# Kernel optimization log

Hardware: AMD Instinct MI355X
Metric: run time of the kernel (lower is better)

## Reference

```python
import jax, jax.numpy as jnp
import numpy as np

B, S, D, H = 2, 2048, 2048, 16
DEPTH = D // H


def setup_inputs() -> dict:
    key = jax.random.key(0)
    ks = jax.random.split(key, 12)
    std = 1.0 / np.sqrt(D)
    mk = lambda k, shape: (jax.random.uniform(k, shape, jnp.float32) * 2 - 1) * std
    # causal additive mask: 1.0 where future position (masked), 0.0 elsewhere
    mask = jnp.triu(jnp.ones((S, S), jnp.float32), k=1)[None, None]
    return {
        "q": jax.random.normal(ks[0], (B, S, D), jnp.float32),
        "k": jax.random.normal(ks[1], (B, S, D), jnp.float32),
        "v": jax.random.normal(ks[2], (B, S, D), jnp.float32),
        "mask": mask,
        "wq_w": mk(ks[3], (D, D)), "wq_b": mk(ks[4], (D,)),
        "wk_w": mk(ks[5], (D, D)), "wk_b": mk(ks[6], (D,)),
        "wv_w": mk(ks[7], (D, D)), "wv_b": mk(ks[8], (D,)),
        "dense_w": mk(ks[9], (D, D)), "dense_b": mk(ks[10], (D,)),
    }


def split_heads(x):
    # [B,S,D] -> [B,H,S,depth]
    b, s, _ = x.shape
    return x.reshape(b, s, H, DEPTH).transpose(0, 2, 1, 3)


def reference(q, k, v, mask, wq_w, wq_b, wk_w, wk_b, wv_w, wv_b, dense_w, dense_b):
    # torch Linear: y = x @ W.T + b
    qh = split_heads(q @ wq_w.T + wq_b)
    kh = split_heads(k @ wk_w.T + wk_b)
    vh = split_heads(v @ wv_w.T + wv_b)
    scale = 1.0 / jnp.sqrt(jnp.asarray(DEPTH, jnp.float32))
    logits = jnp.einsum("bhqd,bhkd->bhqk", qh, kh) * scale
    logits = logits + mask * (-1e9)
    weights = jax.nn.softmax(logits, axis=-1)  # dropout is identity in eval
    out = jnp.einsum("bhqk,bhkd->bhqd", weights, vh)
    out = out.transpose(0, 2, 1, 3).reshape(q.shape[0], -1, D)
    return out @ dense_w.T + dense_b
```

## Files before the change

kernel.cpp:

```cpp
#include <hip/hip_runtime.h>
#include <hip/hip_bf16.h>


typedef __bf16 bf16x8 __attribute__((ext_vector_type(8)));
typedef float f32x4 __attribute__((ext_vector_type(4)));
typedef float f32x16 __attribute__((ext_vector_type(16)));
typedef unsigned short u16;
typedef unsigned int u32;

#define DEV static __device__ __forceinline__

DEV void gload_lds16(const void* g, void* l) {
  __builtin_amdgcn_global_load_lds(
      (const __attribute__((address_space(1))) void*)g,
      (__attribute__((address_space(3))) void*)l, 16, 0, 0);
}

DEV f32x4 mfma16(bf16x8 a, bf16x8 b, f32x4 c) {
  return __builtin_amdgcn_mfma_f32_16x16x32_bf16(a, b, c, 0, 0, 0);
}

DEV f32x16 mfma32(bf16x8 a, bf16x8 b, f32x16 c) {
  return __builtin_amdgcn_mfma_f32_32x32x16_bf16(a, b, c, 0, 0, 0);
}

DEV u16 f2bf(float x) {
  return __builtin_bit_cast(u16, __float2bfloat16(x));
}

DEV u32 pack2(float lo, float hi_) {
  return (u32)f2bf(lo) | ((u32)f2bf(hi_) << 16);
}

#define BAR() __builtin_amdgcn_s_barrier()

__global__ void __launch_bounds__(256) conv_f32_bf16(
    const float* __restrict__ in, u16* __restrict__ out) {
  const size_t i = ((size_t)blockIdx.x * 256 + threadIdx.x) * 4;
  const float4 v = *reinterpret_cast<const float4*>(in + i);
  ushort4 o;
  o.x = f2bf(v.x); o.y = f2bf(v.y); o.z = f2bf(v.z); o.w = f2bf(v.w);
  *reinterpret_cast<ushort4*>(out + i) = o;
}

__global__ void __launch_bounds__(256) conv_all(
    const float* __restrict__ s0, const float* __restrict__ s1,
    const float* __restrict__ s2, const float* __restrict__ s3,
    const float* __restrict__ s4, const float* __restrict__ s5,
    const float* __restrict__ s6,
    u16* __restrict__ d0, u16* __restrict__ d1, u16* __restrict__ d2,
    u16* __restrict__ d3, u16* __restrict__ d4, u16* __restrict__ d5,
    u16* __restrict__ d6, const size_t nact, const size_t nw) {
  const int j = blockIdx.y;
  const size_t i = ((size_t)blockIdx.x * 256 + threadIdx.x) * 4;
  const float* s; u16* d; size_t n;
  switch (j) {
    case 0: s = s0; d = d0; n = nact; break;
    case 1: s = s1; d = d1; n = nact; break;
    case 2: s = s2; d = d2; n = nact; break;
    case 3: s = s3; d = d3; n = nw; break;
    case 4: s = s4; d = d4; n = nw; break;
    case 5: s = s5; d = d5; n = nw; break;
    default: s = s6; d = d6; n = nw; break;
  }
  if (i >= n) return;
  const float4 v = *reinterpret_cast<const float4*>(s + i);
  ushort4 o;
  o.x = f2bf(v.x); o.y = f2bf(v.y); o.z = f2bf(v.z); o.w = f2bf(v.w);
  *reinterpret_cast<ushort4*>(d + i) = o;
}

#define GK 2048

DEV void gemm128_core(const u16* __restrict__ A, const u16* __restrict__ Bw,
                      const float* __restrict__ bias, void* __restrict__ Cout,
                      const int m0, const int n0, const int N,
                      const int out_f32, u16* AsB, u16* BsB) {
  const int tid = threadIdx.x;
  const int lane = tid & 63;
  const int wid = tid >> 6;
  const int wr = wid >> 1, wc = wid & 1;
  const int g = lane >> 4;
  const int r16 = lane & 15;

  int offA[2], offB[2], dstE[2];
#pragma unroll
  for (int rr = 0; rr < 2; ++rr) {
    const int G = rr * 256 + tid;
    const int rp = G >> 3;
    const int s = (G & 7) ^ (rp & 7);
    const int row = rp * 2 + (s >> 2);
    const int ch = s & 3;
    offA[rr] = (m0 + row) * GK + ch * 8;
    offB[rr] = (n0 + row) * GK + ch * 8;
    dstE[rr] = rr * 2048 + wid * 512;
  }

#define STAGE_A(kt, kh) do {                                              \
    u16* base_ = AsB + (((kt) & 1) * 2 + (kh)) * 4096;                    \
    const int go_ = (kt) * 64 + (kh) * 32;                                \
    gload_lds16(A + (size_t)(offA[0] + go_), base_ + dstE[0]);            \
    gload_lds16(A + (size_t)(offA[1] + go_), base_ + dstE[1]);            \
  } while (0)
#define STAGE_B(kt, kh) do {                                              \
    u16* base_ = BsB + (((kt) & 1) * 2 + (kh)) * 4096;                    \
    const int go_ = (kt) * 64 + (kh) * 32;                                \
    gload_lds16(Bw + (size_t)(offB[0] + go_), base_ + dstE[0]);           \
    gload_lds16(Bw + (size_t)(offB[1] + go_), base_ + dstE[1]);           \
  } while (0)
#define READ_A(MH, buf) do {                                              \
    _Pragma("unroll") for (int i_ = 0; i_ < 2; ++i_) {                    \
      const int row_ = wr * 64 + ((MH) * 2 + i_) * 16 + r16;              \
      const int rp_ = row_ >> 1;                                          \
      const int sl_ = (((row_ & 1) << 2) | g) ^ (rp_ & 7);                \
      const int off_ = rp_ * 64 + sl_ * 8;                                \
      af[i_][0] = *(const bf16x8*)(AsB + ((buf) * 2 + 0) * 4096 + off_);  \
      af[i_][1] = *(const bf16x8*)(AsB + ((buf) * 2 + 1) * 4096 + off_);  \
    } } while (0)
#define READ_B(NH, buf, bf) do {                                          \
    _Pragma("unroll") for (int j_ = 0; j_ < 2; ++j_) {                    \
      const int row_ = wc * 64 + ((NH) * 2 + j_) * 16 + r16;              \
      const int rp_ = row_ >> 1;                                          \
      const int sl_ = (((row_ & 1) << 2) | g) ^ (rp_ & 7);                \
      const int off_ = rp_ * 64 + sl_ * 8;                                \
      bf[j_][0] = *(const bf16x8*)(BsB + ((buf) * 2 + 0) * 4096 + off_);  \
      bf[j_][1] = *(const bf16x8*)(BsB + ((buf) * 2 + 1) * 4096 + off_);  \
    } } while (0)
#define MFMA_Q(MH, NH, bf) do {                                           \
    __builtin_amdgcn_s_setprio(1);                                        \
    _Pragma("unroll") for (int i_ = 0; i_ < 2; ++i_)                      \
    _Pragma("unroll") for (int j_ = 0; j_ < 2; ++j_) {                    \
      f32x4 c_ = acc[(MH) * 2 + i_][(NH) * 2 + j_];                       \
      c_ = mfma16(af[i_][0], bf[j_][0], c_);                              \
      c_ = mfma16(af[i_][1], bf[j_][1], c_);                              \
      acc[(MH) * 2 + i_][(NH) * 2 + j_] = c_;                             \
    }                                                                     \
    __builtin_amdgcn_s_setprio(0);                                        \
  } while (0)

  f32x4 acc[4][4];
#pragma unroll
  for (int i = 0; i < 4; ++i)
#pragma unroll
    for (int j = 0; j < 4; ++j) acc[i][j] = {0.f, 0.f, 0.f, 0.f};

  bf16x8 af[2][2], bf0[2][2], bf1[2][2];

  STAGE_B(0, 0); STAGE_B(0, 1); STAGE_A(0, 0); STAGE_A(0, 1);
  STAGE_B(1, 0); STAGE_B(1, 1);
  asm volatile("s_waitcnt vmcnt(4)" ::: "memory");
  BAR();

  for (int it = 0; it < 16; ++it) {
    const bool tail = (it == 15);
    const int t0 = 2 * it, t1 = t0 + 1;
    READ_A(0, 0); READ_B(0, 0, bf0);
    STAGE_A(t1, 0);
    BAR(); MFMA_Q(0, 0, bf0); BAR();
    READ_B(1, 0, bf1);
    STAGE_A(t1, 1);
    BAR(); MFMA_Q(0, 1, bf1); BAR();
    READ_A(1, 0);
    if (!tail) STAGE_B(t0 + 2, 0);
    BAR(); MFMA_Q(1, 0, bf0); BAR();
    if (!tail) {
      STAGE_B(t0 + 2, 1);
      asm volatile("s_waitcnt vmcnt(4)" ::: "memory");
    } else {
      asm volatile("s_waitcnt vmcnt(0)" ::: "memory");
    }
    BAR(); MFMA_Q(1, 1, bf1); BAR();
    READ_A(0, 1); READ_B(0, 1, bf0);
    if (!tail) STAGE_A(t0 + 2, 0);
    BAR(); MFMA_Q(0, 0, bf0); BAR();
    READ_B(1, 1, bf1);
    if (!tail) STAGE_A(t0 + 2, 1);
    BAR(); MFMA_Q(0, 1, bf1); BAR();
    READ_A(1, 1);
    if (!tail) STAGE_B(t1 + 2, 0);
    BAR(); MFMA_Q(1, 0, bf0); BAR();
    if (!tail) {
      STAGE_B(t1 + 2, 1);
      asm volatile("s_waitcnt vmcnt(4)" ::: "memory");
    } else {
      asm volatile("s_waitcnt vmcnt(0)" ::: "memory");
    }
    BAR(); MFMA_Q(1, 1, bf1); BAR();
  }

  const int rbase = m0 + wr * 64 + g * 4;
  const int cb = n0 + wc * 64 + r16;
#pragma unroll
  for (int i = 0; i < 4; ++i) {
#pragma unroll
    for (int j = 0; j < 4; ++j) {
      const int c = cb + j * 16;
      const float bv = bias[c];
#pragma unroll
      for (int r = 0; r < 4; ++r) {
        const float v = acc[i][j][r] + bv;
        const size_t idx = (size_t)(rbase + i * 16 + r) * N + c;
        if (out_f32) ((float*)Cout)[idx] = v;
        else ((u16*)Cout)[idx] = f2bf(v);
      }
    }
  }
#undef STAGE_A
#undef STAGE_B
#undef READ_A
#undef READ_B
#undef MFMA_Q
}

__global__ void __launch_bounds__(256, 2) gemm_qkv3(
    const u16* __restrict__ A0, const u16* __restrict__ A1,
    const u16* __restrict__ A2, const u16* __restrict__ W0,
    const u16* __restrict__ W1, const u16* __restrict__ W2,
    const float* __restrict__ b0, const float* __restrict__ b1,
    const float* __restrict__ b2, u16* __restrict__ C0,
    u16* __restrict__ C1, u16* __restrict__ C2) {
  __shared__ u16 AsB[4 * 4096];
  __shared__ u16 BsB[4 * 4096];
  const int xcd = blockIdx.x & 7;
  const int t = blockIdx.x >> 3;
  const int which = t >> 6;
  const int r = t & 63;
  const int m0 = (xcd * 4 + (r >> 4)) << 7;
  const int n0 = (r & 15) << 7;
  const u16* A = which == 0 ? A0 : which == 1 ? A1 : A2;
  const u16* W = which == 0 ? W0 : which == 1 ? W1 : W2;
  const float* bb = which == 0 ? b0 : which == 1 ? b1 : b2;
  u16* C = which == 0 ? C0 : which == 1 ? C1 : C2;
  gemm128_core(A, W, bb, C, m0, n0, 2048, 0, AsB, BsB);
}

__global__ void __launch_bounds__(256, 2) gemm_one(
    const u16* __restrict__ A, const u16* __restrict__ Bw,
    const float* __restrict__ bias, void* __restrict__ Cout,
    const int out_f32) {
  __shared__ u16 AsB[4 * 4096];
  __shared__ u16 BsB[4 * 4096];
  const int xcd = blockIdx.x & 7;
  const int t = blockIdx.x >> 3;
  const int m0 = (xcd * 4 + (t >> 4)) << 7;
  const int n0 = (t & 15) << 7;
  gemm128_core(A, Bw, bias, Cout, m0, n0, 2048, out_f32, AsB, BsB);
}

#define SEQ 2048
#define DMODEL 2048
#define DH 128
#define QBLK 128
#define KBLK 64
#define C1 0.12751744f
#define THR_RAW 62.73f

__global__ void __launch_bounds__(256, 2) flash_attn(
    const u16* __restrict__ Qh, const u16* __restrict__ Kh,
    const u16* __restrict__ Vh, u16* __restrict__ O) {
  __shared__ u16 Ks[2][KBLK * DH];
  __shared__ u16 Vt[DH * KBLK];

  const int tid = threadIdx.x;
  const int lane = tid & 63;
  const int w = tid >> 6;
  const int hi = lane >> 5;
  const int l31 = lane & 31;

  const int cc = blockIdx.x;
  const int low = cc & 15;
  const int bh = (cc >> 4) & 31;
  const int h = bh & 15;
  const int b = bh >> 4;
  const int g0 = low ^ h;
  const int qt = b ? (15 - g0) : g0;
  const int q0 = qt * QBLK;
  const size_t rowbase = (size_t)b * SEQ;
  const int hoff = h * DH;
  const int qw = q0 + w * 32;
  const int qlane = qw + l31;

  bf16x8 aq[8];
  {
    const u16* qp = &Qh[(rowbase + qlane) * DMODEL + hoff + hi * 8];
#pragma unroll
    for (int c = 0; c < 8; ++c)
      aq[c] = *reinterpret_cast<const bf16x8*>(qp + c * 16);
  }

  f32x16 oacc[4];
#pragma unroll
  for (int dt = 0; dt < 4; ++dt)
#pragma unroll
    for (int r = 0; r < 16; ++r) oacc[dt][r] = 0.f;
  float mrow = -1e30f, lrow = 0.f;

  const int krl = w * 16 + (lane >> 4);
  const int kg4 = w * 4 + (lane >> 4);
  const int du = lane & 15;

  const int nkt = 2 * qt + 2;
  const int ktd = qw >> 6;

  auto stageK = [&](int kt) {
#pragma unroll
    for (int i = 0; i < 4; ++i) {
      const int r = krl + i * 4;
      const int cg = (lane & 15) ^ (r & 15);
      gload_lds16(&Kh[(rowbase + kt * KBLK + r) * DMODEL + hoff + cg * 8],
                  &Ks[kt & 1][(w * 16 + i * 4) * DH]);
    }
  };

  stageK(0);
  uint4 vv[4];
#pragma unroll
  for (int r = 0; r < 4; ++r)
    vv[r] = *reinterpret_cast<const uint4*>(
        &Vh[(rowbase + kg4 * 4 + r) * DMODEL + hoff + du * 8]);

  for (int kt = 0; kt < nkt; ++kt) {
    const int k0 = kt * KBLK;
    if (kt + 1 < nkt) {
      stageK(kt + 1);
      asm volatile("s_waitcnt vmcnt(4)" ::: "memory");
    } else {
      asm volatile("s_waitcnt vmcnt(0)" ::: "memory");
    }

#pragma unroll
    for (int j = 0; j < 8; ++j) {
      const int d = du * 8 + j;
      ushort4 pk4;
      pk4.x = ((const u16*)&vv[0])[j];
      pk4.y = ((const u16*)&vv[1])[j];
      pk4.z = ((const u16*)&vv[2])[j];
      pk4.w = ((const u16*)&vv[3])[j];
      const int slot = (((kg4 >> 1) ^ ((d >> 2) & 7)) * 8) + (kg4 & 1) * 4;
      *reinterpret_cast<ushort4*>(&Vt[d * KBLK + slot]) = pk4;
    }
    asm volatile("s_waitcnt lgkmcnt(0)" ::: "memory");
    BAR();

    const bool active = (kt <= ktd);
    const u16* kb = &Ks[kt & 1][0];
    float p[2][16];
    bool act1 = false;

    if (active) {
      const bool diag = (kt == ktd);
      act1 = (kt < ktd) || (w & 1);
      const bool m0q = diag && !(w & 1);
      const bool m1q = diag && (w & 1);
      {
        f32x16 s;
#pragma unroll
        for (int r = 0; r < 16; ++r) s[r] = 0.f;
        __builtin_amdgcn_s_setprio(1);
#pragma unroll
        for (int c = 0; c < 8; ++c) {
          const int row = l31;
          const bf16x8 kf = *reinterpret_cast<const bf16x8*>(
              &kb[row * DH + (((c * 2 + hi) ^ (row & 15)) * 8)]);
          s = mfma32(kf, aq[c], s);
        }
        __builtin_amdgcn_s_setprio(0);
#pragma unroll
        for (int r = 0; r < 16; ++r) {
          const int krow = (r & 3) + 8 * (r >> 2) + 4 * hi;
          p[0][r] = (m0q && (k0 + krow > qlane)) ? -1e9f : s[r];
        }
      }
      if (act1) {
        f32x16 s;
#pragma unroll
        for (int r = 0; r < 16; ++r) s[r] = 0.f;
        __builtin_amdgcn_s_setprio(1);
#pragma unroll
        for (int c = 0; c < 8; ++c) {
          const int row = 32 + l31;
          const bf16x8 kf = *reinterpret_cast<const bf16x8*>(
              &kb[row * DH + (((c * 2 + hi) ^ (row & 15)) * 8)]);
          s = mfma32(kf, aq[c], s);
        }
        __builtin_amdgcn_s_setprio(0);
#pragma unroll
        for (int r = 0; r < 16; ++r) {
          const int krow = (r & 3) + 8 * (r >> 2) + 4 * hi;
          p[1][r] = (m1q && (k0 + 32 + krow > qlane)) ? -1e9f : s[r];
        }
      } else {
#pragma unroll
        for (int r = 0; r < 16; ++r) p[1][r] = -1e9f;
      }
    }

    if (kt + 1 < nkt) {
#pragma unroll
      for (int r = 0; r < 4; ++r)
        vv[r] = *reinterpret_cast<const uint4*>(
            &Vh[(rowbase + k0 + KBLK + kg4 * 4 + r) * DMODEL + hoff + du * 8]);
    }

    if (active) {
      float mx0 = fmaxf(p[0][0], p[1][0]);
      float mx1 = fmaxf(p[0][1], p[1][1]);
      float mx2 = fmaxf(p[0][2], p[1][2]);
      float mx3 = fmaxf(p[0][3], p[1][3]);
#pragma unroll
      for (int r = 4; r < 16; r += 4) {
        mx0 = fmaxf(mx0, fmaxf(p[0][r + 0], p[1][r + 0]));
        mx1 = fmaxf(mx1, fmaxf(p[0][r + 1], p[1][r + 1]));
        mx2 = fmaxf(mx2, fmaxf(p[0][r + 2], p[1][r + 2]));
        mx3 = fmaxf(mx3, fmaxf(p[0][r + 3], p[1][r + 3]));
      }
      float mx = fmaxf(fmaxf(mx0, mx1), fmaxf(mx2, mx3));
      mx = fmaxf(mx, __shfl_xor(mx, 32));

      const bool need = (mx > mrow + THR_RAW);
      if (__any((int)need)) {
        const float mn = fmaxf(mrow, mx);
        const float al = exp2f((mrow - mn) * C1);
        mrow = mn;
        lrow *= al;
#pragma unroll
        for (int r = 0; r < 16; ++r) {
          const float ar = __shfl(al, (r & 3) + 8 * (r >> 2) + 4 * hi);
#pragma unroll
          for (int dt = 0; dt < 4; ++dt) oacc[dt][r] *= ar;
        }
      }

      float s0 = 0.f, s1 = 0.f, s2 = 0.f, s3 = 0.f;
#pragma unroll
      for (int t = 0; t < 2; ++t)
#pragma unroll
        for (int r = 0; r < 16; r += 4) {
          p[t][r + 0] = exp2f((p[t][r + 0] - mrow) * C1);
          p[t][r + 1] = exp2f((p[t][r + 1] - mrow) * C1);
          p[t][r + 2] = exp2f((p[t][r + 2] - mrow) * C1);
          p[t][r + 3] = exp2f((p[t][r + 3] - mrow) * C1);
          s0 += p[t][r + 0]; s1 += p[t][r + 1];
          s2 += p[t][r + 2]; s3 += p[t][r + 3];
        }
      float sum = (s0 + s1) + (s2 + s3);
      sum += __shfl_xor(sum, 32);
      lrow += sum;

      u32 pk[2][8];
#pragma unroll
      for (int t = 0; t < 2; ++t)
#pragma unroll
        for (int m = 0; m < 8; ++m)
          pk[t][m] = pack2(p[t][2 * m], p[t][2 * m + 1]);

      __builtin_amdgcn_s_setprio(1);
#pragma unroll
      for (int ks = 0; ks < 4; ++ks) {
        if (ks >= 2 && !act1) break;
        const int t = ks >> 1;
        const int bs = (ks & 1) * 4;
        const u32 q0s = __shfl_xor(pk[t][bs + 0], 32);
        const u32 q1s = __shfl_xor(pk[t][bs + 1], 32);
        const u32 q2s = __shfl_xor(pk[t][bs + 2], 32);
        const u32 q3s = __shfl_xor(pk[t][bs + 3], 32);
        union { u32 u[4]; bf16x8 v; } pa;
        pa.u[0] = hi ? q2s : pk[t][bs + 0];
        pa.u[1] = hi ? q3s : pk[t][bs + 1];
        pa.u[2] = hi ? pk[t][bs + 2] : q0s;
        pa.u[3] = hi ? pk[t][bs + 3] : q1s;
#pragma unroll
        for (int dt = 0; dt < 4; ++dt) {
          const int d = dt * 32 + l31;
          const bf16x8 vf = *reinterpret_cast<const bf16x8*>(
              &Vt[d * KBLK + (((ks * 2 + hi) ^ ((d >> 2) & 7)) * 8)]);
          oacc[dt] = mfma32(pa.v, vf, oacc[dt]);
        }
      }
      __builtin_amdgcn_s_setprio(0);
    }

    BAR();
  }

  const float li = __builtin_amdgcn_rcpf(lrow);
#pragma unroll
  for (int r = 0; r < 16; ++r) {
    const int rowq = (r & 3) + 8 * (r >> 2) + 4 * hi;
    const float lr = __shfl(li, rowq);
    u16* op = &O[(rowbase + qw + rowq) * DMODEL + hoff + l31];
#pragma unroll
    for (int dt = 0; dt < 4; ++dt) op[dt * 32] = f2bf(oacc[dt][r] * lr);
  }
}

extern "C" void kernel_launch(void* const* d_in, const int* in_sizes, int n_in,
                              void* d_out, int out_size, void* d_ws,
                              size_t ws_size, hipStream_t stream) {
  const int Bv = 2, S = 2048, D = 2048;
  const int M = Bv * S;
  const size_t NT = (size_t)M * D;
  const size_t NW = (size_t)D * D;

  const float* q = (const float*)d_in[0];
  const float* k = (const float*)d_in[1];
  const float* v = (const float*)d_in[2];
  const float* wq_w = (const float*)d_in[4];
  const float* wq_b = (const float*)d_in[5];
  const float* wk_w = (const float*)d_in[6];
  const float* wk_b = (const float*)d_in[7];
  const float* wv_w = (const float*)d_in[8];
  const float* wv_b = (const float*)d_in[9];
  const float* dw = (const float*)d_in[10];
  const float* db = (const float*)d_in[11];
  float* out = (float*)d_out;

  const dim3 blk(256);
  const dim3 gattn(512);
  const size_t need = (7 * NT + 4 * NW) * 2;

  if (ws_size >= need) {
    u16* base = (u16*)d_ws;
    u16* Xq = base;
    u16* Xk = Xq + NT;
    u16* Xv = Xk + NT;
    u16* Wq = Xv + NT;
    u16* Wk = Wq + NW;
    u16* Wv = Wk + NW;
    u16* Wd = Wv + NW;
    u16* Qh = Wd + NW;
    u16* Kh = Qh + NT;
    u16* Vh = Kh + NT;
    u16* Obf = Vh + NT;

    conv_all<<<dim3((unsigned)(NT / 1024), 7), blk, 0, stream>>>(
        q, k, v, wq_w, wk_w, wv_w, dw, Xq, Xk, Xv, Wq, Wk, Wv, Wd, NT, NW);
    gemm_qkv3<<<dim3(1536), blk, 0, stream>>>(
        Xq, Xk, Xv, Wq, Wk, Wv, wq_b, wk_b, wv_b, Qh, Kh, Vh);
    flash_attn<<<gattn, blk, 0, stream>>>(Qh, Kh, Vh, Obf);
    gemm_one<<<dim3(512), blk, 0, stream>>>(Obf, Wd, db, out, 1);
  } else {
    u16* Xbf = (u16*)d_ws;
    u16* Wbf = Xbf + NT;
    u16* Qh = Wbf + NW;
    u16* Kh = Qh + NT;
    u16* Vh = Kh + NT;
    u16* Obf = Vh + NT;
    const dim3 gact((unsigned)(NT / 1024));
    const dim3 gw((unsigned)(NW / 1024));

    conv_f32_bf16<<<gact, blk, 0, stream>>>(q, Xbf);
    conv_f32_bf16<<<gw, blk, 0, stream>>>(wq_w, Wbf);
    gemm_one<<<dim3(512), blk, 0, stream>>>(Xbf, Wbf, wq_b, Qh, 0);
    conv_f32_bf16<<<gact, blk, 0, stream>>>(k, Xbf);
    conv_f32_bf16<<<gw, blk, 0, stream>>>(wk_w, Wbf);
    gemm_one<<<dim3(512), blk, 0, stream>>>(Xbf, Wbf, wk_b, Kh, 0);
    conv_f32_bf16<<<gact, blk, 0, stream>>>(v, Xbf);
    conv_f32_bf16<<<gw, blk, 0, stream>>>(wv_w, Wbf);
    gemm_one<<<dim3(512), blk, 0, stream>>>(Xbf, Wbf, wv_b, Vh, 0);
    flash_attn<<<gattn, blk, 0, stream>>>(Qh, Kh, Vh, Obf);
    conv_f32_bf16<<<gw, blk, 0, stream>>>(dw, Wbf);
    gemm_one<<<dim3(512), blk, 0, stream>>>(Obf, Wbf, db, out, 1);
  }
}
```

Before: 298.3 us.

## Restructure GEMM main loop into two coarser phases per k-tile

Replaces the four-quadrant schedule of each k-tile (eight barrier pairs per iteration) with two half-tile phases: all four B fragments and half of the A fragments are read, then 16 MFMAs are issued between each barrier pair. Global-to-LDS staging is grouped in pairs to match. This halves the number of barriers and gives each MFMA burst more work, at the cost of more live B-fragment registers and fewer interleaving points for hiding LDS and global loads.

Result: faster. 289.4 us (-3.0%).

```diff
diff --git a/kernel.cpp b/kernel.cpp
--- a/kernel.cpp
+++ b/kernel.cpp
@@ -108,7 +108,7 @@
     gload_lds16(Bw + (size_t)(offB[0] + go_), base_ + dstE[0]);           \
     gload_lds16(Bw + (size_t)(offB[1] + go_), base_ + dstE[1]);           \
   } while (0)
-#define READ_A(MH, buf) do {                                              \
+#define READ_A2(MH, buf) do {                                             \
     _Pragma("unroll") for (int i_ = 0; i_ < 2; ++i_) {                    \
       const int row_ = wr * 64 + ((MH) * 2 + i_) * 16 + r16;              \
       const int rp_ = row_ >> 1;                                          \
@@ -117,23 +117,23 @@
       af[i_][0] = *(const bf16x8*)(AsB + ((buf) * 2 + 0) * 4096 + off_);  \
       af[i_][1] = *(const bf16x8*)(AsB + ((buf) * 2 + 1) * 4096 + off_);  \
     } } while (0)
-#define READ_B(NH, buf, bf) do {                                          \
-    _Pragma("unroll") for (int j_ = 0; j_ < 2; ++j_) {                    \
-      const int row_ = wc * 64 + ((NH) * 2 + j_) * 16 + r16;              \
+#define READ_B4(buf) do {                                                 \
+    _Pragma("unroll") for (int j_ = 0; j_ < 4; ++j_) {                    \
+      const int row_ = wc * 64 + j_ * 16 + r16;                           \
       const int rp_ = row_ >> 1;                                          \
       const int sl_ = (((row_ & 1) << 2) | g) ^ (rp_ & 7);                \
       const int off_ = rp_ * 64 + sl_ * 8;                                \
       bf[j_][0] = *(const bf16x8*)(BsB + ((buf) * 2 + 0) * 4096 + off_);  \
       bf[j_][1] = *(const bf16x8*)(BsB + ((buf) * 2 + 1) * 4096 + off_);  \
     } } while (0)
-#define MFMA_Q(MH, NH, bf) do {                                           \
+#define MFMA16(MH) do {                                                   \
     __builtin_amdgcn_s_setprio(1);                                        \
     _Pragma("unroll") for (int i_ = 0; i_ < 2; ++i_)                      \
-    _Pragma("unroll") for (int j_ = 0; j_ < 2; ++j_) {                    \
-      f32x4 c_ = acc[(MH) * 2 + i_][(NH) * 2 + j_];                       \
+    _Pragma("unroll") for (int j_ = 0; j_ < 4; ++j_) {                    \
+      f32x4 c_ = acc[(MH) * 2 + i_][j_];                                  \
       c_ = mfma16(af[i_][0], bf[j_][0], c_);                              \
       c_ = mfma16(af[i_][1], bf[j_][1], c_);                              \
-      acc[(MH) * 2 + i_][(NH) * 2 + j_] = c_;                             \
+      acc[(MH) * 2 + i_][j_] = c_;                                        \
     }                                                                     \
     __builtin_amdgcn_s_setprio(0);                                        \
   } while (0)
@@ -144,7 +144,7 @@
 #pragma unroll
     for (int j = 0; j < 4; ++j) acc[i][j] = {0.f, 0.f, 0.f, 0.f};
 
-  bf16x8 af[2][2], bf0[2][2], bf1[2][2];
+  bf16x8 af[2][2], bf[4][2];
 
   STAGE_B(0, 0); STAGE_B(0, 1); STAGE_A(0, 0); STAGE_A(0, 1);
   STAGE_B(1, 0); STAGE_B(1, 1);
@@ -153,39 +153,30 @@
 
   for (int it = 0; it < 16; ++it) {
     const bool tail = (it == 15);
-    const int t0 = 2 * it, t1 = t0 + 1;
-    READ_A(0, 0); READ_B(0, 0, bf0);
-    STAGE_A(t1, 0);
-    BAR(); MFMA_Q(0, 0, bf0); BAR();
-    READ_B(1, 0, bf1);
-    STAGE_A(t1, 1);
-    BAR(); MFMA_Q(0, 1, bf1); BAR();
-    READ_A(1, 0);
-    if (!tail) STAGE_B(t0 + 2, 0);
-    BAR(); MFMA_Q(1, 0, bf0); BAR();
+    const int T = 2 * it;
+    const int b0 = T & 1, b1 = (T + 1) & 1;
+    READ_A2(0, b0); READ_B4(b0);
+    STAGE_A(T + 1, 0); STAGE_A(T + 1, 1);
+    BAR(); MFMA16(0); BAR();
+    READ_A2(1, b0);
     if (!tail) {
-      STAGE_B(t0 + 2, 1);
+      STAGE_B(T + 2, 0); STAGE_B(T + 2, 1);
       asm volatile("s_waitcnt vmcnt(4)" ::: "memory");
     } else {
       asm volatile("s_waitcnt vmcnt(0)" ::: "memory");
     }
-    BAR(); MFMA_Q(1, 1, bf1); BAR();
-    READ_A(0, 1); READ_B(0, 1, bf0);
-    if (!tail) STAGE_A(t0 + 2, 0);
-    BAR(); MFMA_Q(0, 0, bf0); BAR();
-    READ_B(1, 1, bf1);
-    if (!tail) STAGE_A(t0 + 2, 1);
-    BAR(); MFMA_Q(0, 1, bf1); BAR();
-    READ_A(1, 1);
-    if (!tail) STAGE_B(t1 + 2, 0);
-    BAR(); MFMA_Q(1, 0, bf0); BAR();
+    BAR(); MFMA16(1); BAR();
+    READ_A2(0, b1); READ_B4(b1);
+    if (!tail) { STAGE_A(T + 2, 0); STAGE_A(T + 2, 1); }
+    BAR(); MFMA16(0); BAR();
+    READ_A2(1, b1);
     if (!tail) {
-      STAGE_B(t1 + 2, 1);
+      STAGE_B(T + 3, 0); STAGE_B(T + 3, 1);
       asm volatile("s_waitcnt vmcnt(4)" ::: "memory");
     } else {
       asm volatile("s_waitcnt vmcnt(0)" ::: "memory");
     }
-    BAR(); MFMA_Q(1, 1, bf1); BAR();
+    BAR(); MFMA16(1); BAR();
   }
 
   const int rbase = m0 + wr * 64 + g * 4;
@@ -207,9 +198,9 @@
   }
 #undef STAGE_A
 #undef STAGE_B
-#undef READ_A
-#undef READ_B
-#undef MFMA_Q
+#undef READ_A2
+#undef READ_B4
+#undef MFMA16
 }
 
 __global__ void __launch_bounds__(256, 2) gemm_qkv3(
```
